# Optimization experiments

Hardware: AMD Instinct MI355X
Metric: run time of the kernel (lower is better)

The kernel has to match this reference:

```python
import jax, jax.numpy as jnp
import numpy as np

BETA = 0.25
NUM_EMBEDDINGS = 2048
EMBEDDING_DIM = 512
N_TOKENS = 32768


def setup_inputs() -> dict:
    key = jax.random.key(0)
    k_z, k_e = jax.random.split(key)
    z = jax.random.normal(k_z, (N_TOKENS, EMBEDDING_DIM), dtype=jnp.float32)
    # nn.Embedding weight init: uniform(-1/K, 1/K)
    lim = 1.0 / NUM_EMBEDDINGS
    embedding = jax.random.uniform(
        k_e, (NUM_EMBEDDINGS, EMBEDDING_DIM), dtype=jnp.float32,
        minval=-lim, maxval=lim)
    return {"z": z, "embedding": embedding}


def reference(z, embedding):
    # z: [N, D], embedding: [K, D]
    z = z.reshape(-1, EMBEDDING_DIM)
    # squared euclidean distance: ||z||^2 + ||e||^2 - 2 z e^T  -> [N, K]
    d = (jnp.sum(z * z, axis=1, keepdims=True)
         + jnp.sum(embedding * embedding, axis=1)
         - 2.0 * jnp.matmul(z, embedding.T))
    min_encoding_indices = jnp.argmin(d, axis=1)[:, None]          # [N, 1]
    z_q = embedding[min_encoding_indices[:, 0]]                    # [N, D] gather

    sg = jax.lax.stop_gradient
    loss = jnp.mean((sg(z_q) - z) ** 2) + BETA * jnp.mean((z_q - sg(z)) ** 2)

    # straight-through estimator
    z_q_st = z + sg(z_q - z)

    # avg_probs = mean of one-hot encodings == normalized code-usage histogram
    n = z.shape[0]
    counts = jnp.zeros((NUM_EMBEDDINGS,), dtype=z.dtype).at[
        min_encoding_indices[:, 0]].add(1.0)
    avg_probs = counts / n
    perplexity = jnp.exp(-jnp.sum(avg_probs * jnp.log(avg_probs + 1e-10)))

    return (z_q_st, min_encoding_indices, loss, perplexity)
```

## Files before the change

kernel.cpp:

```cpp
#include <hip/hip_runtime.h>
#include <hip/hip_bf16.h>

#define N_TOK 32768
#define DIM   512
#define NE    2048

#define IDX_OFF  (N_TOK * DIM)
#define LOSS_OFF (IDX_OFF + N_TOK)
#define PERP_OFF (LOSS_OFF + 1)

#define KB(x) ((size_t)(x) << 10)
#define EPS 4e-4f
#define EPS_SEL 1e-3f

typedef __attribute__((ext_vector_type(8))) short bf16x8;
typedef __attribute__((ext_vector_type(4))) float f32x4;

__device__ inline unsigned short f2bf(float f) {
  unsigned int x = __float_as_uint(f);
  x = x + 0x7fffu + ((x >> 16) & 1u);
  return (unsigned short)(x >> 16);
}
__device__ inline float bfround(float f) {
  return __uint_as_float((unsigned int)f2bf(f) << 16);
}

__global__ __launch_bounds__(256) void npsum_cvt_all(
    const float* __restrict__ z, const float* __restrict__ e,
    float* __restrict__ zsum, float* __restrict__ esum,
    unsigned short* __restrict__ zbf, unsigned short* __restrict__ ebf,
    int* __restrict__ counts) {
#pragma clang fp contract(off)
  const int bz = blockIdx.x;
  if (bz < 8) counts[bz * 256 + threadIdx.x] = 0;
  const bool isz = bz < (N_TOK / 16);
  const int blk = isz ? bz : bz - (N_TOK / 16);
  const float* x = isz ? z : e;
  float* outs = isz ? zsum : esum;
  unsigned short* xbf = isz ? zbf : ebf;

  int wave = threadIdx.x >> 6;
  int lane = threadIdx.x & 63;
  int grp = lane >> 4, l = lane & 15;
  int row = blk * 16 + wave * 4 + grp;
  {
    const float* a = x + (size_t)row * DIM;
    float L[4];
    #pragma unroll
    for (int b = 0; b < 4; ++b) {
      const float* p = a + b * 128 + l;
      float q[8];
      #pragma unroll
      for (int j = 0; j < 8; ++j) {
        float t = p[16 * j];
        float s = t * t;
        asm volatile("" : "+v"(s));
        q[j] = s;
      }
      float v = ((q[0] + q[1]) + (q[2] + q[3])) + ((q[4] + q[5]) + (q[6] + q[7]));
      v += __shfl_xor(v, 8);
      v += __shfl_xor(v, 4);
      v += __shfl_xor(v, 2);
      v += __shfl_xor(v, 1);
      L[b] = v;
    }
    if (l == 0) outs[row] = (L[0] + L[1]) + (L[2] + L[3]);
  }
  const float* blkp = x + (size_t)blk * 16 * DIM;
  unsigned short* ob = xbf + (size_t)blk * 16 * DIM;
  #pragma unroll
  for (int u = 0; u < 4; ++u) {
    size_t off = (size_t)(u * 256 + threadIdx.x) * 8;
    float4 a2 = *(const float4*)(blkp + off);
    float4 b2 = *(const float4*)(blkp + off + 4);
    unsigned short h[8] = {f2bf(a2.x), f2bf(a2.y), f2bf(a2.z), f2bf(a2.w),
                           f2bf(b2.x), f2bf(b2.y), f2bf(b2.z), f2bf(b2.w)};
    *(uint4*)(ob + off) = *(uint4*)h;
  }
}

__device__ inline void stage_half(const unsigned short* __restrict__ gsrc,
                                  unsigned short* lds, int w, int l) {
  const int swz_col = ((l & 7) ^ (l >> 3)) * 8;
  const int rsub = l >> 3;
  #pragma unroll
  for (int s4 = 0; s4 < 2; ++s4) {
    int s = w * 2 + s4;
    const unsigned short* g = gsrc + (size_t)(s * 8 + rsub) * DIM + swz_col;
    __builtin_amdgcn_global_load_lds(
        (const __attribute__((address_space(1))) unsigned int*)g,
        (__attribute__((address_space(3))) unsigned int*)(lds + s * 512),
        16, 0, 0);
  }
}

#define BAR()   asm volatile("s_barrier" ::: "memory")
#define VMCNT4  asm volatile("s_waitcnt vmcnt(4)" ::: "memory")
#define VMCNT0  asm volatile("s_waitcnt vmcnt(0)" ::: "memory")

__global__ __launch_bounds__(512, 2) void gemm_groupmin(
    const unsigned short* __restrict__ ebf, const unsigned short* __restrict__ zbf,
    const float* __restrict__ esum, unsigned* __restrict__ gmv) {
  extern __shared__ unsigned short smem[];
  unsigned short* As = smem;
  unsigned short* Bs = smem + 32768;

  const int tid = threadIdx.x;
  const int tb = blockIdx.x;
  const int cb = blockIdx.y;
  const int w = tid >> 6, l = tid & 63;
  const int lr = l & 15, lk = l >> 4;
  const int wrow = (w >> 2) * 128;
  const int wcol = (w & 3) * 64;

  f32x4 acc[8][4];
  #pragma unroll
  for (int i = 0; i < 8; ++i)
    #pragma unroll
    for (int j = 0; j < 4; ++j) acc[i][j] = (f32x4)(0.f);

  bf16x8 aR[8], bA[4], bB[4];

  const unsigned short* Ag = ebf + (size_t)(cb * 256) * DIM;
  const unsigned short* Bg = zbf + (size_t)(tb * 256) * DIM;

#define LOADA(slot, qm) do { \
  _Pragma("unroll") for (int i2 = 0; i2 < 4; ++i2) { \
    int R = wrow + (qm)*64 + i2*16 + lr; \
    int rbase = ((slot)*2 + (R>>7))*8192 + (R&127)*64; \
    aR[i2*2+0] = *(const bf16x8*)&As[rbase + (((lk    ) ^ (R&7))*8)]; \
    aR[i2*2+1] = *(const bf16x8*)&As[rbase + (((4 + lk) ^ (R&7))*8)]; \
  } } while (0)

#define LOADB(dst, slot, qn) do { \
  _Pragma("unroll") for (int j = 0; j < 2; ++j) { \
    int C = wcol + (qn)*32 + j*16 + lr; \
    int cbase = ((slot)*2 + (C>>7))*8192 + (C&127)*64; \
    dst[j*2+0] = *(const bf16x8*)&Bs[cbase + (((lk    ) ^ (C&7))*8)]; \
    dst[j*2+1] = *(const bf16x8*)&Bs[cbase + (((4 + lk) ^ (C&7))*8)]; \
  } } while (0)

#define MFMA16(qm, qn, bX) do { \
  __builtin_amdgcn_s_setprio(1); \
  _Pragma("unroll") for (int i2 = 0; i2 < 4; ++i2) \
    _Pragma("unroll") for (int j = 0; j < 2; ++j) { \
      acc[(qm)*4+i2][(qn)*2+j] = __builtin_amdgcn_mfma_f32_16x16x32_bf16( \
          aR[i2*2+0], bX[j*2+0], acc[(qm)*4+i2][(qn)*2+j], 0, 0, 0); \
      acc[(qm)*4+i2][(qn)*2+j] = __builtin_amdgcn_mfma_f32_16x16x32_bf16( \
          aR[i2*2+1], bX[j*2+1], acc[(qm)*4+i2][(qn)*2+j], 0, 0, 0); \
    } \
  __builtin_amdgcn_s_setprio(0); \
} while (0)

  stage_half(Bg,                 Bs,             w, l);
  stage_half(Bg + 128 * DIM,     Bs + 8192,      w, l);
  stage_half(Ag,                 As,             w, l);
  stage_half(Ag + 128 * DIM,     As + 8192,      w, l);
  stage_half(Bg + 64,            Bs + 2 * 8192,  w, l);
  stage_half(Bg + 128 * DIM + 64, Bs + 3 * 8192, w, l);
  VMCNT4;
  BAR();

  #pragma unroll
  for (int i = 0; i < 4; ++i) {
    const int t1k = (2 * i + 1) * 64;
    const int u0k = (2 * i + 2) * 64;
    const int u1k = (2 * i + 3) * 64;
    LOADA(0, 0); LOADB(bA, 0, 0); LOADB(bB, 0, 1);
    stage_half(Ag + t1k, As + 2 * 8192, w, l);
    BAR(); MFMA16(0, 0, bA);
    stage_half(Ag + 128 * DIM + t1k, As + 3 * 8192, w, l);
    BAR(); MFMA16(0, 1, bB);
    LOADA(0, 1);
    if (i < 3) stage_half(Bg + u0k, Bs, w, l);
    BAR(); MFMA16(1, 0, bA);
    if (i < 3) stage_half(Bg + 128 * DIM + u0k, Bs + 8192, w, l);
    BAR(); MFMA16(1, 1, bB);
    if (i < 3) { VMCNT4; } else { VMCNT0; }
    BAR();
    LOADA(1, 0); LOADB(bA, 1, 0); LOADB(bB, 1, 1);
    if (i < 3) stage_half(Ag + u0k, As, w, l);
    BAR(); MFMA16(0, 0, bA);
    if (i < 3) stage_half(Ag + 128 * DIM + u0k, As + 8192, w, l);
    BAR(); MFMA16(0, 1, bB);
    LOADA(1, 1);
    if (i < 3) stage_half(Bg + u1k, Bs + 2 * 8192, w, l);
    BAR(); MFMA16(1, 0, bA);
    if (i < 3) stage_half(Bg + 128 * DIM + u1k, Bs + 3 * 8192, w, l);
    BAR(); MFMA16(1, 1, bB);
    if (i < 3) { VMCNT4; BAR(); }
  }

  float esr[8][4];
  #pragma unroll
  for (int i = 0; i < 8; ++i)
    #pragma unroll
    for (int q = 0; q < 4; ++q)
      esr[i][q] = esum[cb * 256 + wrow + i * 16 + lk * 4 + q];

  unsigned gmv8[4][8];
  #pragma unroll
  for (int i = 0; i < 8; ++i) {
    #pragma unroll
    for (int j = 0; j < 4; ++j) {
      float v0 = fmaf(-2.f, acc[i][j][0], esr[i][0]);
      float v1 = fmaf(-2.f, acc[i][j][1], esr[i][1]);
      float v2 = fmaf(-2.f, acc[i][j][2], esr[i][2]);
      float v3 = fmaf(-2.f, acc[i][j][3], esr[i][3]);
      float m = fminf(fminf(v0, v1), fminf(v2, v3));
      m = fminf(m, __shfl_xor(m, 16));
      m = fminf(m, __shfl_xor(m, 32));
      float gl = m + EPS;
      int mk = (((v0 <= gl) ? 1 : 0) | ((v1 <= gl) ? 2 : 0) |
                ((v2 <= gl) ? 4 : 0) | ((v3 <= gl) ? 8 : 0)) << (lk * 4);
      mk |= __shfl_xor(mk, 16);
      mk |= __shfl_xor(mk, 32);
      gmv8[j][i] = ((unsigned)f2bf(m) << 16) | (unsigned)(mk & 0xFFFF);
    }
  }
  if (lk == 0) {
    #pragma unroll
    for (int j = 0; j < 4; ++j) {
      int token = tb * 256 + wcol + j * 16 + lr;
      size_t gb = (size_t)token * 128 + cb * 16 + (w >> 2) * 8;
      uint4 q0 = {gmv8[j][0], gmv8[j][1], gmv8[j][2], gmv8[j][3]};
      uint4 q1 = {gmv8[j][4], gmv8[j][5], gmv8[j][6], gmv8[j][7]};
      *(uint4*)&gmv[gb] = q0;
      *(uint4*)&gmv[gb + 4] = q1;
    }
  }
#undef LOADA
#undef LOADB
#undef MFMA16
}

__global__ __launch_bounds__(256) void select_exact(
    const float* __restrict__ z, const float* __restrict__ e,
    const float* __restrict__ zsum, const float* __restrict__ esum,
    const unsigned* __restrict__ gmv,
    int* __restrict__ idx_final, int* __restrict__ counts,
    float* __restrict__ out, float* __restrict__ lossp, int fused) {
  __shared__ float lred[4];
  const int wid = threadIdx.x >> 6;
  const int t = blockIdx.x * 4 + wid;
  const int lane = threadIdx.x & 63;
  const float* zr = z + (size_t)t * DIM;

  float4 za = *(const float4*)(zr + lane * 4);
  float4 zb = *(const float4*)(zr + 256 + lane * 4);

  unsigned u0 = gmv[(size_t)t * 128 + lane];
  unsigned u1 = gmv[(size_t)t * 128 + 64 + lane];
  float g0 = __uint_as_float(u0 & 0xFFFF0000u);
  float g1 = __uint_as_float(u1 & 0xFFFF0000u);
  float m = fminf(g0, g1);
  #pragma unroll
  for (int s = 32; s >= 1; s >>= 1) m = fminf(m, __shfl_xor(m, s));
  float lim = m + EPS_SEL;
  unsigned long long mm0 = __ballot(g0 <= lim);
  unsigned long long mm1 = __ballot(g1 <= lim);
  float zst = zsum[t];
  float bd = 3.402823466e38f; int bc = 0x7fffffff;

  #pragma unroll 1
  for (int half = 0; half < 2; ++half) {
    unsigned long long mk = half ? mm1 : mm0;
    while (mk) {
      int b = __ffsll((unsigned long long)mk) - 1;
      mk &= mk - 1;
      const int base = (half * 64 + b) * 16;
      unsigned gm = (unsigned)__shfl((int)(half ? u1 : u0), b) & 0xFFFFu;
      while (gm) {
        int ci = __ffs(gm) - 1;
        gm &= gm - 1;
        int c = base + ci;
        const float* er = e + (size_t)c * DIM;
        float4 ea = *(const float4*)(er + lane * 4);
        float4 eb = *(const float4*)(er + 256 + lane * 4);
        float p = 0.f;
        p = fmaf(za.x, ea.x, p); p = fmaf(za.y, ea.y, p);
        p = fmaf(za.z, ea.z, p); p = fmaf(za.w, ea.w, p);
        p = fmaf(zb.x, eb.x, p); p = fmaf(zb.y, eb.y, p);
        p = fmaf(zb.z, eb.z, p); p = fmaf(zb.w, eb.w, p);
        #pragma unroll
        for (int s = 1; s <= 32; s <<= 1) p += __shfl_xor(p, s);
        float d = (zst + esum[c]) - 2.f * p;
        if (d < bd) { bd = d; bc = c; }
      }
    }
  }
  if (fused) {
    const float* er = e + (size_t)(bc & (NE - 1)) * DIM;
    float4 ea = *(const float4*)(er + lane * 4);
    float4 eb = *(const float4*)(er + 256 + lane * 4);
    float* op = out + (size_t)t * DIM;
    float4 oa, ob;
    oa.x = bfround(ea.x); oa.y = bfround(ea.y);
    oa.z = bfround(ea.z); oa.w = bfround(ea.w);
    ob.x = bfround(eb.x); ob.y = bfround(eb.y);
    ob.z = bfround(eb.z); ob.w = bfround(eb.w);
    *(float4*)(op + lane * 4) = oa;
    *(float4*)(op + 256 + lane * 4) = ob;
  }
  if (lane == 0) {
    idx_final[t] = bc;
    out[IDX_OFF + t] = bfround((float)bc);
    atomicAdd(&counts[bc], 1);
    lred[wid] = bd;
  }
  __syncthreads();
  if (threadIdx.x == 0)
    lossp[blockIdx.x] = (lred[0] + lred[1]) + (lred[2] + lred[3]);
}

__device__ inline void finalize_body(const int* __restrict__ counts,
                                     const float* __restrict__ lossp,
                                     float* __restrict__ out) {
  __shared__ float red[4], red2[4];
  int tid = threadIdx.x;
  float s = 0.f;
  for (int j = tid; j < NE; j += 256) {
    float p = (float)counts[j] * (1.0f / (float)N_TOK);
    s += p * logf(p + 1e-10f);
  }
  float ls = 0.f;
  for (int j = tid; j < N_TOK / 4; j += 256) ls += lossp[j];
  #pragma unroll
  for (int m = 32; m >= 1; m >>= 1) {
    s += __shfl_xor(s, m);
    ls += __shfl_xor(ls, m);
  }
  if ((tid & 63) == 0) { red[tid >> 6] = s; red2[tid >> 6] = ls; }
  __syncthreads();
  if (tid == 0) {
    float tot = red[0] + red[1] + red[2] + red[3];
    float lt = red2[0] + red2[1] + red2[2] + red2[3];
    out[PERP_OFF] = bfround(expf(-tot));
    out[LOSS_OFF] = bfround(lt * 1.25f / (float)(N_TOK * DIM));
  }
}

__global__ __launch_bounds__(256) void fin_only(
    const int* __restrict__ counts, const float* __restrict__ lossp,
    float* __restrict__ out) {
  finalize_body(counts, lossp, out);
}

__global__ __launch_bounds__(256) void scatter_fin(
    const float* __restrict__ e, const int* __restrict__ idx_final,
    const int* __restrict__ counts, const float* __restrict__ lossp,
    float* __restrict__ out) {
  if (blockIdx.x == N_TOK / 8) { finalize_body(counts, lossp, out); return; }
  int t = blockIdx.x * 8 + (threadIdx.x >> 5);
  int g = threadIdx.x & 31;
  int idx = idx_final[t] & (NE - 1);
  const float* er = e + (size_t)idx * DIM;
  float* op = out + (size_t)t * DIM;
  #pragma unroll
  for (int p = 0; p < 4; ++p) {
    int c = p * 128 + g * 4;
    float4 ev = *(const float4*)(er + c);
    float4 ov;
    ov.x = bfround(ev.x); ov.y = bfround(ev.y);
    ov.z = bfround(ev.z); ov.w = bfround(ev.w);
    *(float4*)(op + c) = ov;
  }
}

extern "C" void kernel_launch(void* const* d_in, const int* in_sizes, int n_in,
                              void* d_out, int out_size, void* d_ws, size_t ws_size,
                              hipStream_t stream) {
  const float* z = (const float*)d_in[0];
  const float* e = (const float*)d_in[1];
  float* out = (float*)d_out;
  char* ws = (char*)d_ws;

  float*    zsum      = (float*)(ws + KB(0));
  float*    esum      = (float*)(ws + KB(128));
  int*      counts    = (int*)(ws + KB(136));
  float*    lossp     = (float*)(ws + KB(144));
  int*      idx_final = (int*)(ws + KB(176));
  unsigned short* ebf = (unsigned short*)(ws + KB(304));

  unsigned short* zbf = (unsigned short*)out;

  const size_t gmv_off = KB(2368);
  const size_t gmv_bytes = (size_t)N_TOK * 128 * 4;
  const bool fused = ws_size >= gmv_off + gmv_bytes;
  unsigned* gmv = fused ? (unsigned*)(ws + gmv_off)
                        : (unsigned*)(out + 8388608);

  npsum_cvt_all<<<N_TOK / 16 + NE / 16, 256, 0, stream>>>(
      z, e, zsum, esum, zbf, ebf, counts);
  gemm_groupmin<<<dim3(N_TOK / 256, NE / 256), 512, 131072, stream>>>(
      ebf, zbf, esum, gmv);
  select_exact<<<N_TOK / 4, 256, 0, stream>>>(z, e, zsum, esum, gmv,
                                              idx_final, counts, out, lossp,
                                              fused ? 1 : 0);
  if (fused) {
    fin_only<<<1, 256, 0, stream>>>(counts, lossp, out);
  } else {
    scatter_fin<<<N_TOK / 8 + 1, 256, 0, stream>>>(e, idx_final, counts, lossp, out);
  }
}
```

Before: 156.6 us.

## Place bf16 z and group-min scratch inside output rows, always take fused path

The bf16 copy of z and the per-token group-min scratch now live inside each token's row of the output buffer. Each 2048-byte row holds 512 bytes of group-min words, then 1024 bytes of bf16 z, which the GEMM reads with a doubled row stride. The select kernel always gathers and writes z_q itself, so the workspace-size check, the idx_final buffer and the separate scatter kernel are removed. This means no extra scatter pass when the workspace is small, and each token's scratch sits in the same row it later overwrites. The cost is a strided B-operand load in the GEMM and reliance on in-row ordering: each wave reads its scratch before writing z_q over it.

New measurement: 160.8 us. 2.7% more time.

```diff
diff --git a/kernel.cpp b/kernel.cpp
--- a/kernel.cpp
+++ b/kernel.cpp
@@ -12,6 +12,7 @@
 #define KB(x) ((size_t)(x) << 10)
 #define EPS 4e-4f
 #define EPS_SEL 1e-3f
+
 
 typedef __attribute__((ext_vector_type(8))) short bf16x8;
 typedef __attribute__((ext_vector_type(4))) float f32x4;
@@ -28,7 +29,7 @@
 __global__ __launch_bounds__(256) void npsum_cvt_all(
     const float* __restrict__ z, const float* __restrict__ e,
     float* __restrict__ zsum, float* __restrict__ esum,
-    unsigned short* __restrict__ zbf, unsigned short* __restrict__ ebf,
+    float* __restrict__ out, unsigned short* __restrict__ ebf,
     int* __restrict__ counts) {
 #pragma clang fp contract(off)
   const int bz = blockIdx.x;
@@ -37,7 +38,6 @@
   const int blk = isz ? bz : bz - (N_TOK / 16);
   const float* x = isz ? z : e;
   float* outs = isz ? zsum : esum;
-  unsigned short* xbf = isz ? zbf : ebf;
 
   int wave = threadIdx.x >> 6;
   int lane = threadIdx.x & 63;
@@ -67,7 +67,6 @@
     if (l == 0) outs[row] = (L[0] + L[1]) + (L[2] + L[3]);
   }
   const float* blkp = x + (size_t)blk * 16 * DIM;
-  unsigned short* ob = xbf + (size_t)blk * 16 * DIM;
   #pragma unroll
   for (int u = 0; u < 4; ++u) {
     size_t off = (size_t)(u * 256 + threadIdx.x) * 8;
@@ -75,18 +74,25 @@
     float4 b2 = *(const float4*)(blkp + off + 4);
     unsigned short h[8] = {f2bf(a2.x), f2bf(a2.y), f2bf(a2.z), f2bf(a2.w),
                            f2bf(b2.x), f2bf(b2.y), f2bf(b2.z), f2bf(b2.w)};
-    *(uint4*)(ob + off) = *(uint4*)h;
+    if (isz) {
+      int r = (int)(off >> 9), c = (int)(off & 511);
+      unsigned short* rp = (unsigned short*)((char*)out +
+          (size_t)(blk * 16 + r) * 2048 + 512);
+      *(uint4*)(rp + c) = *(uint4*)h;
+    } else {
+      *(uint4*)(ebf + off + (size_t)blk * 16 * DIM) = *(uint4*)h;
+    }
   }
 }
 
 __device__ inline void stage_half(const unsigned short* __restrict__ gsrc,
-                                  unsigned short* lds, int w, int l) {
+                                  unsigned short* lds, int w, int l, int rstride) {
   const int swz_col = ((l & 7) ^ (l >> 3)) * 8;
   const int rsub = l >> 3;
   #pragma unroll
   for (int s4 = 0; s4 < 2; ++s4) {
     int s = w * 2 + s4;
-    const unsigned short* g = gsrc + (size_t)(s * 8 + rsub) * DIM + swz_col;
+    const unsigned short* g = gsrc + (size_t)(s * 8 + rsub) * rstride + swz_col;
     __builtin_amdgcn_global_load_lds(
         (const __attribute__((address_space(1))) unsigned int*)g,
         (__attribute__((address_space(3))) unsigned int*)(lds + s * 512),
@@ -99,8 +105,8 @@
 #define VMCNT0  asm volatile("s_waitcnt vmcnt(0)" ::: "memory")
 
 __global__ __launch_bounds__(512, 2) void gemm_groupmin(
-    const unsigned short* __restrict__ ebf, const unsigned short* __restrict__ zbf,
-    const float* __restrict__ esum, unsigned* __restrict__ gmv) {
+    const unsigned short* __restrict__ ebf, float* __restrict__ out,
+    const float* __restrict__ esum) {
   extern __shared__ unsigned short smem[];
   unsigned short* As = smem;
   unsigned short* Bs = smem + 32768;
@@ -122,7 +128,8 @@
   bf16x8 aR[8], bA[4], bB[4];
 
   const unsigned short* Ag = ebf + (size_t)(cb * 256) * DIM;
-  const unsigned short* Bg = zbf + (size_t)(tb * 256) * DIM;
+  const unsigned short* Bg = (const unsigned short*)((const char*)out +
+      (size_t)(tb * 256) * 2048 + 512);
 
 #define LOADA(slot, qm) do { \
   _Pragma("unroll") for (int i2 = 0; i2 < 4; ++i2) { \
@@ -152,12 +159,12 @@
   __builtin_amdgcn_s_setprio(0); \
 } while (0)
 
-  stage_half(Bg,                 Bs,             w, l);
-  stage_half(Bg + 128 * DIM,     Bs + 8192,      w, l);
-  stage_half(Ag,                 As,             w, l);
-  stage_half(Ag + 128 * DIM,     As + 8192,      w, l);
-  stage_half(Bg + 64,            Bs + 2 * 8192,  w, l);
-  stage_half(Bg + 128 * DIM + 64, Bs + 3 * 8192, w, l);
+  stage_half(Bg,                  Bs,            w, l, 1024);
+  stage_half(Bg + 128 * 1024,     Bs + 8192,     w, l, 1024);
+  stage_half(Ag,                  As,            w, l, 512);
+  stage_half(Ag + 128 * DIM,      As + 8192,     w, l, 512);
+  stage_half(Bg + 64,             Bs + 2 * 8192, w, l, 1024);
+  stage_half(Bg + 128 * 1024 + 64, Bs + 3 * 8192, w, l, 1024);
   VMCNT4;
   BAR();
 
@@ -167,26 +174,26 @@
     const int u0k = (2 * i + 2) * 64;
     const int u1k = (2 * i + 3) * 64;
     LOADA(0, 0); LOADB(bA, 0, 0); LOADB(bB, 0, 1);
-    stage_half(Ag + t1k, As + 2 * 8192, w, l);
+    stage_half(Ag + t1k, As + 2 * 8192, w, l, 512);
     BAR(); MFMA16(0, 0, bA);
-    stage_half(Ag + 128 * DIM + t1k, As + 3 * 8192, w, l);
+    stage_half(Ag + 128 * DIM + t1k, As + 3 * 8192, w, l, 512);
     BAR(); MFMA16(0, 1, bB);
     LOADA(0, 1);
-    if (i < 3) stage_half(Bg + u0k, Bs, w, l);
+    if (i < 3) stage_half(Bg + u0k, Bs, w, l, 1024);
     BAR(); MFMA16(1, 0, bA);
-    if (i < 3) stage_half(Bg + 128 * DIM + u0k, Bs + 8192, w, l);
+    if (i < 3) stage_half(Bg + 128 * 1024 + u0k, Bs + 8192, w, l, 1024);
     BAR(); MFMA16(1, 1, bB);
     if (i < 3) { VMCNT4; } else { VMCNT0; }
     BAR();
     LOADA(1, 0); LOADB(bA, 1, 0); LOADB(bB, 1, 1);
-    if (i < 3) stage_half(Ag + u0k, As, w, l);
+    if (i < 3) stage_half(Ag + u0k, As, w, l, 512);
     BAR(); MFMA16(0, 0, bA);
-    if (i < 3) stage_half(Ag + 128 * DIM + u0k, As + 8192, w, l);
+    if (i < 3) stage_half(Ag + 128 * DIM + u0k, As + 8192, w, l, 512);
     BAR(); MFMA16(0, 1, bB);
     LOADA(1, 1);
-    if (i < 3) stage_half(Bg + u1k, Bs + 2 * 8192, w, l);
+    if (i < 3) stage_half(Bg + u1k, Bs + 2 * 8192, w, l, 1024);
     BAR(); MFMA16(1, 0, bA);
-    if (i < 3) stage_half(Bg + 128 * DIM + u1k, Bs + 3 * 8192, w, l);
+    if (i < 3) stage_half(Bg + 128 * 1024 + u1k, Bs + 3 * 8192, w, l, 1024);
     BAR(); MFMA16(1, 1, bB);
     if (i < 3) { VMCNT4; BAR(); }
   }
@@ -222,11 +229,12 @@
     #pragma unroll
     for (int j = 0; j < 4; ++j) {
       int token = tb * 256 + wcol + j * 16 + lr;
-      size_t gb = (size_t)token * 128 + cb * 16 + (w >> 2) * 8;
+      unsigned* gr = (unsigned*)((char*)out + (size_t)token * 2048);
+      int gofs = cb * 16 + (w >> 2) * 8;
       uint4 q0 = {gmv8[j][0], gmv8[j][1], gmv8[j][2], gmv8[j][3]};
       uint4 q1 = {gmv8[j][4], gmv8[j][5], gmv8[j][6], gmv8[j][7]};
-      *(uint4*)&gmv[gb] = q0;
-      *(uint4*)&gmv[gb + 4] = q1;
+      *(uint4*)&gr[gofs] = q0;
+      *(uint4*)&gr[gofs + 4] = q1;
     }
   }
 #undef LOADA
@@ -237,9 +245,8 @@
 __global__ __launch_bounds__(256) void select_exact(
     const float* __restrict__ z, const float* __restrict__ e,
     const float* __restrict__ zsum, const float* __restrict__ esum,
-    const unsigned* __restrict__ gmv,
-    int* __restrict__ idx_final, int* __restrict__ counts,
-    float* __restrict__ out, float* __restrict__ lossp, int fused) {
+    int* __restrict__ counts, float* __restrict__ out,
+    float* __restrict__ lossp) {
   __shared__ float lred[4];
   const int wid = threadIdx.x >> 6;
   const int t = blockIdx.x * 4 + wid;
@@ -249,8 +256,9 @@
   float4 za = *(const float4*)(zr + lane * 4);
   float4 zb = *(const float4*)(zr + 256 + lane * 4);
 
-  unsigned u0 = gmv[(size_t)t * 128 + lane];
-  unsigned u1 = gmv[(size_t)t * 128 + 64 + lane];
+  const unsigned* gr = (const unsigned*)((const char*)out + (size_t)t * 2048);
+  unsigned u0 = gr[lane];
+  unsigned u1 = gr[64 + lane];
   float g0 = __uint_as_float(u0 & 0xFFFF0000u);
   float g1 = __uint_as_float(u1 & 0xFFFF0000u);
   float m = fminf(g0, g1);
@@ -289,7 +297,7 @@
       }
     }
   }
-  if (fused) {
+  {
     const float* er = e + (size_t)(bc & (NE - 1)) * DIM;
     float4 ea = *(const float4*)(er + lane * 4);
     float4 eb = *(const float4*)(er + 256 + lane * 4);
@@ -303,7 +311,6 @@
     *(float4*)(op + 256 + lane * 4) = ob;
   }
   if (lane == 0) {
-    idx_final[t] = bc;
     out[IDX_OFF + t] = bfround((float)bc);
     atomicAdd(&counts[bc], 1);
     lred[wid] = bd;
@@ -313,9 +320,9 @@
     lossp[blockIdx.x] = (lred[0] + lred[1]) + (lred[2] + lred[3]);
 }
 
-__device__ inline void finalize_body(const int* __restrict__ counts,
-                                     const float* __restrict__ lossp,
-                                     float* __restrict__ out) {
+__global__ __launch_bounds__(256) void fin_only(
+    const int* __restrict__ counts, const float* __restrict__ lossp,
+    float* __restrict__ out) {
   __shared__ float red[4], red2[4];
   int tid = threadIdx.x;
   float s = 0.f;
@@ -340,33 +347,6 @@
   }
 }
 
-__global__ __launch_bounds__(256) void fin_only(
-    const int* __restrict__ counts, const float* __restrict__ lossp,
-    float* __restrict__ out) {
-  finalize_body(counts, lossp, out);
-}
-
-__global__ __launch_bounds__(256) void scatter_fin(
-    const float* __restrict__ e, const int* __restrict__ idx_final,
-    const int* __restrict__ counts, const float* __restrict__ lossp,
-    float* __restrict__ out) {
-  if (blockIdx.x == N_TOK / 8) { finalize_body(counts, lossp, out); return; }
-  int t = blockIdx.x * 8 + (threadIdx.x >> 5);
-  int g = threadIdx.x & 31;
-  int idx = idx_final[t] & (NE - 1);
-  const float* er = e + (size_t)idx * DIM;
-  float* op = out + (size_t)t * DIM;
-  #pragma unroll
-  for (int p = 0; p < 4; ++p) {
-    int c = p * 128 + g * 4;
-    float4 ev = *(const float4*)(er + c);
-    float4 ov;
-    ov.x = bfround(ev.x); ov.y = bfround(ev.y);
-    ov.z = bfround(ev.z); ov.w = bfround(ev.w);
-    *(float4*)(op + c) = ov;
-  }
-}
-
 extern "C" void kernel_launch(void* const* d_in, const int* in_sizes, int n_in,
                               void* d_out, int out_size, void* d_ws, size_t ws_size,
                               hipStream_t stream) {
@@ -375,31 +355,17 @@
   float* out = (float*)d_out;
   char* ws = (char*)d_ws;
 
-  float*    zsum      = (float*)(ws + KB(0));
-  float*    esum      = (float*)(ws + KB(128));
-  int*      counts    = (int*)(ws + KB(136));
-  float*    lossp     = (float*)(ws + KB(144));
-  int*      idx_final = (int*)(ws + KB(176));
-  unsigned short* ebf = (unsigned short*)(ws + KB(304));
-
-  unsigned short* zbf = (unsigned short*)out;
-
-  const size_t gmv_off = KB(2368);
-  const size_t gmv_bytes = (size_t)N_TOK * 128 * 4;
-  const bool fused = ws_size >= gmv_off + gmv_bytes;
-  unsigned* gmv = fused ? (unsigned*)(ws + gmv_off)
-                        : (unsigned*)(out + 8388608);
+  float*    zsum   = (float*)(ws + KB(0));
+  float*    esum   = (float*)(ws + KB(128));
+  int*      counts = (int*)(ws + KB(136));
+  float*    lossp  = (float*)(ws + KB(144));
+  unsigned short* ebf = (unsigned short*)(ws + KB(176));
 
   npsum_cvt_all<<<N_TOK / 16 + NE / 16, 256, 0, stream>>>(
-      z, e, zsum, esum, zbf, ebf, counts);
+      z, e, zsum, esum, out, ebf, counts);
   gemm_groupmin<<<dim3(N_TOK / 256, NE / 256), 512, 131072, stream>>>(
-      ebf, zbf, esum, gmv);
-  select_exact<<<N_TOK / 4, 256, 0, stream>>>(z, e, zsum, esum, gmv,
-                                              idx_final, counts, out, lossp,
-                                              fused ? 1 : 0);
-  if (fused) {
-    fin_only<<<1, 256, 0, stream>>>(counts, lossp, out);
-  } else {
-    scatter_fin<<<N_TOK / 8 + 1, 256, 0, stream>>>(e, idx_final, counts, lossp, out);
-  }
-}
+      ebf, out, esum);
+  select_exact<<<N_TOK / 4, 256, 0, stream>>>(z, e, zsum, esum,
+                                              counts, out, lossp);
+  fin_only<<<1, 256, 0, stream>>>(counts, lossp, out);
+}
```
